# Optimization experiments

Measured on AMD Instinct MI355X. Metric: run time of the kernel, lower is better.

Reference implementation:

```python
import jax, jax.numpy as jnp
import numpy as np

B, C = 16, 256          # batch, feature_dim
P, K = 20, 50           # max_polygons, max_points
H4 = W4 = 32            # p4 spatial
H2 = W2 = 128           # p2 spatial


def setup_inputs() -> dict:
    key = jax.random.key(0)
    ks = jax.random.split(key, 12)

    def w(k, shape, fan_in):
        return jax.random.normal(k, shape, jnp.float32) * (1.0 / np.sqrt(fan_in))

    return {
        "p4": jax.random.normal(ks[0], (B, C, H4, W4), jnp.float32),
        "p2": jax.random.normal(ks[1], (B, C, H2, W2), jnp.float32),
        "segmentation": jax.random.uniform(ks[2], (B, 1, H2, W2), dtype=jnp.float32),
        # init_net linears (torch layout: [out, in])
        "W1": w(ks[3], (1024, C * 64), C * 64), "b1": jnp.zeros((1024,), jnp.float32),
        "W2": w(ks[4], (P * K * 2, 1024), 1024), "b2": jnp.zeros((P * K * 2,), jnp.float32),
        # refine_net
        "R1": w(ks[5], (128, C + 2), C + 2), "rb1": jnp.zeros((128,), jnp.float32),
        "R2": w(ks[6], (64, 128), 128), "rb2": jnp.zeros((64,), jnp.float32),
        "R3": w(ks[7], (2, 64), 64), "rb3": jnp.zeros((2,), jnp.float32),
        # validity_net
        "V1": w(ks[8], (128, K * 2), K * 2), "vb1": jnp.zeros((128,), jnp.float32),
        "V2": w(ks[9], (1, 128), 128), "vb2": jnp.zeros((1,), jnp.float32),
    }


def _bilinear_sample(img, xy):
    """F.grid_sample(align_corners=False, padding='zeros') for one image.
    img: [C, H, W]; xy: [N, 2] in [-1, 1] with xy[:, 0]=x (width), xy[:, 1]=y (height).
    Returns [N, C]."""
    Cc, H, W = img.shape
    x = ((xy[:, 0] + 1.0) * W - 1.0) * 0.5
    y = ((xy[:, 1] + 1.0) * H - 1.0) * 0.5
    x0 = jnp.floor(x)
    y0 = jnp.floor(y)
    wx1 = x - x0
    wy1 = y - y0

    def corner(xi, yi, wgt):
        valid = (xi >= 0) & (xi <= W - 1) & (yi >= 0) & (yi <= H - 1)
        xc = jnp.clip(xi, 0, W - 1).astype(jnp.int32)
        yc = jnp.clip(yi, 0, H - 1).astype(jnp.int32)
        v = img[:, yc, xc]  # [C, N]
        return v * (wgt * valid.astype(img.dtype))[None, :]

    out = (corner(x0, y0, (1 - wx1) * (1 - wy1))
           + corner(x0 + 1, y0, wx1 * (1 - wy1))
           + corner(x0, y0 + 1, (1 - wx1) * wy1)
           + corner(x0 + 1, y0 + 1, wx1 * wy1))
    return out.T  # [N, C]


def reference(p4, p2, segmentation, W1, b1, W2, b2, R1, rb1, R2, rb2, R3, rb3, V1, vb1, V2, vb2):
    Bn, Cc, h4, w4 = p4.shape
    pooled = p4.reshape(Bn, Cc, 8, h4 // 8, 8, w4 // 8).mean(axis=(3, 5))
    flat = pooled.reshape(Bn, -1)                       # [B, C*64]
    h = jax.nn.relu(flat @ W1.T + b1)
    init_pts = jax.nn.sigmoid(h @ W2.T + b2).reshape(Bn, P, K, 2)

    # refine: grid_sample point gather + 3-layer MLP
    grid = init_pts * 2.0 - 1.0                          # [B, P, K, 2]
    xy = grid.reshape(Bn, -1, 2)                         # [B, N=P*K, 2]
    sampled = jax.vmap(_bilinear_sample)(p2, xy)         # [B, N, C]
    coords = init_pts.reshape(Bn, -1, 2)
    feat = jnp.concatenate([sampled, coords], axis=-1)   # [B, N, C+2]
    h1 = jax.nn.relu(feat @ R1.T + rb1)
    h2 = jax.nn.relu(h1 @ R2.T + rb2)
    disp = jnp.tanh(h2 @ R3.T + rb3).reshape(Bn, P, K, 2)
    refined = jnp.clip(init_pts + 0.1 * disp, 0.0, 1.0)

    # validity
    pf = refined.reshape(Bn * P, K * 2)
    v = jax.nn.sigmoid(jax.nn.relu(pf @ V1.T + vb1) @ V2.T + vb2).reshape(Bn, P)
    return refined, v, init_pts
```

## Files before the change

### kernel.cpp

```cpp
#include <hip/hip_runtime.h>
#include <hip/hip_bf16.h>
#include <math.h>

#define NB 16
#define NC 256
#define NPTS 1000
#define NN2 2000
#define D1 1024
#define KFLAT 16384

typedef unsigned short ushort8 __attribute__((ext_vector_type(8)));

static __device__ __forceinline__ float bf2f(unsigned short v) {
    union { unsigned int u; float f; } x;
    x.u = ((unsigned int)v) << 16;
    return x.f;
}

__global__ __launch_bounds__(256) void k_prep(const float* __restrict__ R1,
                                              const float* __restrict__ V1,
                                              float* __restrict__ R1t,
                                              float* __restrict__ V1t_g) {
    int idx = blockIdx.x * 256 + threadIdx.x;
    if (idx < 33024) {
        int j = idx / 258, k = idx % 258;
        R1t[k * 128 + j] = R1[idx];
    } else if (idx < 33024 + 12800) {
        int t = idx - 33024;
        int j = t / 100, k = t % 100;
        V1t_g[k * 128 + j] = V1[t];
    }
}

__global__ __launch_bounds__(256) void k_pool(const float* __restrict__ p4,
                                              __hip_bfloat16* __restrict__ flat_bf) {
    int o = blockIdx.x * 256 + threadIdx.x;
    int bc = o >> 6;
    int ij = o & 63;
    int i = ij >> 3, j = ij & 7;
    const float* src = p4 + ((size_t)bc * 32 + i * 4) * 32 + j * 4;
    float s = 0.f;
#pragma unroll
    for (int di = 0; di < 4; ++di) {
        float4 v = *reinterpret_cast<const float4*>(src + di * 32);
        s += v.x + v.y + v.z + v.w;
    }
    flat_bf[o] = __float2bfloat16(s * (1.0f / 16.0f));
}

__global__ __launch_bounds__(512) void k_fc1(const __hip_bfloat16* __restrict__ flat_bf,
                                             const float* __restrict__ W1,
                                             const float* __restrict__ b1,
                                             float* __restrict__ h) {
    __shared__ unsigned short tile[2 * 16 * 512];
    __shared__ float red[8 * 16];
    const int tid = threadIdx.x;
    const int wave = tid >> 6, lane = tid & 63;
    const int colw = wave & 3, half = wave >> 2;
    const int n = blockIdx.x * 4 + colw;
    float acc[16];
#pragma unroll
    for (int m = 0; m < 16; ++m) acc[m] = 0.f;
    const float4* W1r4 = reinterpret_cast<const float4*>(W1 + (size_t)n * KFLAT + half * 8192);
    const ushort8* flat8 = reinterpret_cast<const ushort8*>(flat_bf);
    ushort8* tile8 = reinterpret_cast<ushort8*>(tile);

    float4 wa = W1r4[lane * 2], wb = W1r4[lane * 2 + 1];
    for (int it = 0; it < 16; ++it) {
        __syncthreads();
#pragma unroll
        for (int r = 0; r < 4; ++r) {
            int idx = tid + r * 512;
            int hh = idx >> 10, m = (idx >> 6) & 15, off = idx & 63;
            tile8[idx] = flat8[m * 2048 + hh * 1024 + it * 64 + off];
        }
        __syncthreads();
        float4 na = wa, nb = wb;
        if (it < 15) {
            na = W1r4[(it + 1) * 128 + lane * 2];
            nb = W1r4[(it + 1) * 128 + lane * 2 + 1];
        }
#pragma unroll
        for (int m = 0; m < 16; ++m) {
            ushort8 u = tile8[half * 1024 + m * 64 + lane];
            float s = wa.x * bf2f(u.s0) + wa.y * bf2f(u.s1)
                    + wa.z * bf2f(u.s2) + wa.w * bf2f(u.s3)
                    + wb.x * bf2f(u.s4) + wb.y * bf2f(u.s5)
                    + wb.z * bf2f(u.s6) + wb.w * bf2f(u.s7);
            acc[m] += s;
        }
        wa = na; wb = nb;
    }
#pragma unroll
    for (int m = 0; m < 16; ++m) {
        float v = acc[m];
#pragma unroll
        for (int off = 32; off > 0; off >>= 1) v += __shfl_xor(v, off, 64);
        acc[m] = v;
    }
    __syncthreads();
    if (lane == 0) {
#pragma unroll
        for (int m = 0; m < 16; ++m) red[wave * 16 + m] = acc[m];
    }
    __syncthreads();
    if (tid < 64) {
        int c = tid >> 4, m = tid & 15;
        float v = red[c * 16 + m] + red[(c + 4) * 16 + m] + b1[blockIdx.x * 4 + c];
        h[m * D1 + blockIdx.x * 4 + c] = fmaxf(v, 0.f);
    }
}

__global__ __launch_bounds__(256) void k_fc2(const float* __restrict__ h,
                                             const float* __restrict__ W2,
                                             const float* __restrict__ b2,
                                             float* __restrict__ init_ws,
                                             float* __restrict__ out_init) {
    const int tid = threadIdx.x;
    const int wave = tid >> 6, lane = tid & 63;
    const int n = blockIdx.x * 4 + wave;
    float acc[16];
#pragma unroll
    for (int m = 0; m < 16; ++m) acc[m] = 0.f;
    const float4* W2r = reinterpret_cast<const float4*>(W2 + (size_t)n * D1);
    const float4* h4  = reinterpret_cast<const float4*>(h);
#pragma unroll
    for (int it = 0; it < 4; ++it) {
        int k4 = it * 64 + lane;
        float4 w = W2r[k4];
#pragma unroll
        for (int m = 0; m < 16; ++m) {
            float4 f = h4[m * 256 + k4];
            acc[m] += w.x * f.x + w.y * f.y + w.z * f.z + w.w * f.w;
        }
    }
    float bias = b2[n];
#pragma unroll
    for (int m = 0; m < 16; ++m) {
        float v = acc[m];
#pragma unroll
        for (int off = 32; off > 0; off >>= 1) v += __shfl_xor(v, off, 64);
        if (lane == 0) {
            float s = 1.f / (1.f + expf(-(v + bias)));
            init_ws[m * NN2 + n] = s;
            out_init[m * NN2 + n] = s;
        }
    }
}

__global__ __launch_bounds__(1024) void k_sample(const float* __restrict__ p2,
                                                 const float* __restrict__ init_ws,
                                                 __hip_bfloat16* __restrict__ sampled) {
    __shared__ float img[128 * 128];
    const int bc = blockIdx.x;
    const int b = bc >> 8;
    const float4* src4 = reinterpret_cast<const float4*>(p2 + (size_t)bc * 16384);
    float4* dst4 = reinterpret_cast<float4*>(img);
#pragma unroll
    for (int i = 0; i < 4; ++i)
        dst4[threadIdx.x + i * 1024] = src4[threadIdx.x + i * 1024];
    __syncthreads();
    const float* ip = init_ws + b * NN2;
    const int n = threadIdx.x;
    if (n < NPTS) {
        float2 sxy = *reinterpret_cast<const float2*>(ip + 2 * n);
        float x = sxy.x * 128.f - 0.5f;
        float y = sxy.y * 128.f - 0.5f;
        float x0f = floorf(x), y0f = floorf(y);
        float wx = x - x0f, wy = y - y0f;
        int x0 = (int)x0f, y0 = (int)y0f;
        int x1 = x0 + 1, y1 = y0 + 1;
        bool vx0 = (x0 >= 0) && (x0 <= 127);
        bool vx1 = (x1 >= 0) && (x1 <= 127);
        bool vy0 = (y0 >= 0) && (y0 <= 127);
        bool vy1 = (y1 >= 0) && (y1 <= 127);
        int cx0 = min(max(x0, 0), 127), cx1 = min(max(x1, 0), 127);
        int cy0 = min(max(y0, 0), 127), cy1 = min(max(y1, 0), 127);
        float v00 = (vx0 && vy0) ? img[cy0 * 128 + cx0] : 0.f;
        float v10 = (vx1 && vy0) ? img[cy0 * 128 + cx1] : 0.f;
        float v01 = (vx0 && vy1) ? img[cy1 * 128 + cx0] : 0.f;
        float v11 = (vx1 && vy1) ? img[cy1 * 128 + cx1] : 0.f;
        float r = v00 * (1.f - wx) * (1.f - wy) + v10 * wx * (1.f - wy)
                + v01 * (1.f - wx) * wy + v11 * wx * wy;
        sampled[(size_t)bc * NPTS + n] = __float2bfloat16(r);
    }
}

__global__ __launch_bounds__(256) void k_r1(const __hip_bfloat16* __restrict__ sampled,
                                            const float* __restrict__ init_ws,
                                            const float* __restrict__ R1t,
                                            const float* __restrict__ rb1,
                                            float* __restrict__ h1t) {
    __shared__ float As[64][128];
    __shared__ float Bs[64][32];
    const int tid = threadIdx.x;
    const int b = blockIdx.x >> 5;
    const int n0 = (blockIdx.x & 31) * 32;
    const int nt = tid & 15;
    const int jt = tid >> 4;
    float acc[8][2];
#pragma unroll
    for (int a = 0; a < 8; ++a) { acc[a][0] = 0.f; acc[a][1] = 0.f; }

    for (int k0 = 0; k0 < 256; k0 += 64) {
        __syncthreads();
        for (int idx = tid; idx < 128 * 64; idx += 256) {
            int kk = idx >> 7, r = idx & 127;
            As[kk][r] = R1t[(k0 + kk) * 128 + r];
        }
        for (int idx = tid; idx < 64 * 32; idx += 256) {
            int r = idx >> 5, col = idx & 31;
            int n = n0 + col;
            Bs[r][col] = (n < NPTS)
                ? __bfloat162float(sampled[((size_t)(b * 256 + k0 + r)) * NPTS + n])
                : 0.f;
        }
        __syncthreads();
#pragma unroll 8
        for (int kk = 0; kk < 64; ++kk) {
            float4 a0 = *reinterpret_cast<const float4*>(&As[kk][jt * 4]);
            float4 a1 = *reinterpret_cast<const float4*>(&As[kk][64 + jt * 4]);
            float2 bb = *reinterpret_cast<const float2*>(&Bs[kk][nt * 2]);
            float av[8] = {a0.x, a0.y, a0.z, a0.w, a1.x, a1.y, a1.z, a1.w};
#pragma unroll
            for (int a = 0; a < 8; ++a) {
                acc[a][0] += av[a] * bb.x;
                acc[a][1] += av[a] * bb.y;
            }
        }
    }
    const int npair = n0 + nt * 2;
    float4 c4 = make_float4(0.f, 0.f, 0.f, 0.f);
    if (npair < NPTS)
        c4 = *reinterpret_cast<const float4*>(init_ws + b * NN2 + 2 * npair);
#pragma unroll
    for (int a = 0; a < 8; ++a) {
        int j = (a < 4) ? (jt * 4 + a) : (64 + jt * 4 + (a - 4));
        float rx = R1t[256 * 128 + j];
        float ry = R1t[257 * 128 + j];
        float bj = rb1[j];
        float v0 = fmaxf(acc[a][0] + rx * c4.x + ry * c4.y + bj, 0.f);
        float v1 = fmaxf(acc[a][1] + rx * c4.z + ry * c4.w + bj, 0.f);
        if (npair < NPTS) {
            float2 st = make_float2(v0, v1);
            *reinterpret_cast<float2*>(h1t + ((size_t)(b * 128 + j)) * NPTS + npair) = st;
        }
    }
}

__global__ __launch_bounds__(512) void k_r23(const float* __restrict__ h1t,
                                             const float* __restrict__ init_ws,
                                             const float* __restrict__ R2,
                                             const float* __restrict__ rb2,
                                             const float* __restrict__ R3,
                                             const float* __restrict__ rb3,
                                             float* __restrict__ refined) {
    __shared__ float hbuf[128][64];
    __shared__ float part[8][2][64];
    const int tid = threadIdx.x;
    const int wave = tid >> 6, lane = tid & 63;
    const int b = blockIdx.x >> 4;
    const int n0 = (blockIdx.x & 15) * 64;
    const int nc = min(n0 + lane, NPTS - 1);

    const float* hsrc = h1t + (size_t)b * (128 * NPTS) + nc;
#pragma unroll
    for (int i = 0; i < 16; ++i) {
        int r = wave * 16 + i;
        hbuf[r][lane] = hsrc[(size_t)r * NPTS];
    }
    __syncthreads();

    const int jb = __builtin_amdgcn_readfirstlane(wave * 8);
    float acc[8];
#pragma unroll
    for (int jj = 0; jj < 8; ++jj) acc[jj] = rb2[jb + jj];
#pragma unroll 4
    for (int k = 0; k < 128; ++k) {
        float hv = hbuf[k][lane];
#pragma unroll
        for (int jj = 0; jj < 8; ++jj)
            acc[jj] = fmaf(R2[(jb + jj) * 128 + k], hv, acc[jj]);
    }
    float d0 = 0.f, d1 = 0.f;
#pragma unroll
    for (int jj = 0; jj < 8; ++jj) {
        float a = fmaxf(acc[jj], 0.f);
        d0 = fmaf(R3[jb + jj], a, d0);
        d1 = fmaf(R3[64 + jb + jj], a, d1);
    }
    part[wave][0][lane] = d0;
    part[wave][1][lane] = d1;
    __syncthreads();
    if (tid < 64) {
        float s0 = 0.f, s1 = 0.f;
#pragma unroll
        for (int w = 0; w < 8; ++w) { s0 += part[w][0][tid]; s1 += part[w][1][tid]; }
        float2 ip = *reinterpret_cast<const float2*>(init_ws + b * NN2 + 2 * nc);
        float rx = fminf(fmaxf(ip.x + 0.1f * tanhf(s0 + rb3[0]), 0.f), 1.f);
        float ry = fminf(fmaxf(ip.y + 0.1f * tanhf(s1 + rb3[1]), 0.f), 1.f);
        if (n0 + tid < NPTS) {
            *reinterpret_cast<float2*>(refined + ((size_t)b * NPTS + n0 + tid) * 2)
                = make_float2(rx, ry);
        }
    }
}

__global__ __launch_bounds__(256) void k_vhead(const float* __restrict__ refined,
                                               const float* __restrict__ V1t_g,
                                               const float* __restrict__ vb1,
                                               const float* __restrict__ V2,
                                               const float* __restrict__ vb2,
                                               float* __restrict__ vout) {
    __shared__ float V1t[100][128];
    __shared__ float pf[4][100];
    const int tid = threadIdx.x, wave = tid >> 6, lane = tid & 63;
    for (int idx = tid; idx < 100 * 128; idx += 256)
        V1t[idx >> 7][idx & 127] = V1t_g[idx];
    __syncthreads();
    const int row = blockIdx.x * 4 + wave;
    const float* src = refined + row * 100;
    if (lane < 50) {
        pf[wave][lane] = src[lane];
        pf[wave][lane + 50] = src[lane + 50];
    }
    __syncthreads();
    float a0 = vb1[lane], a1 = vb1[64 + lane];
#pragma unroll 10
    for (int k = 0; k < 100; ++k) {
        float p = pf[wave][k];
        a0 += V1t[k][lane] * p;
        a1 += V1t[k][64 + lane] * p;
    }
    float s = fmaxf(a0, 0.f) * V2[lane] + fmaxf(a1, 0.f) * V2[64 + lane];
#pragma unroll
    for (int off = 32; off > 0; off >>= 1) s += __shfl_xor(s, off, 64);
    if (lane == 0) vout[row] = 1.f / (1.f + expf(-(s + vb2[0])));
}

extern "C" void kernel_launch(void* const* d_in, const int* in_sizes, int n_in,
                              void* d_out, int out_size, void* d_ws, size_t ws_size,
                              hipStream_t stream) {
    const float* p4  = (const float*)d_in[0];
    const float* p2  = (const float*)d_in[1];
    const float* W1  = (const float*)d_in[3];
    const float* b1  = (const float*)d_in[4];
    const float* W2  = (const float*)d_in[5];
    const float* b2  = (const float*)d_in[6];
    const float* R1  = (const float*)d_in[7];
    const float* rb1 = (const float*)d_in[8];
    const float* R2  = (const float*)d_in[9];
    const float* rb2 = (const float*)d_in[10];
    const float* R3  = (const float*)d_in[11];
    const float* rb3 = (const float*)d_in[12];
    const float* V1  = (const float*)d_in[13];
    const float* vb1 = (const float*)d_in[14];
    const float* V2  = (const float*)d_in[15];
    const float* vb2 = (const float*)d_in[16];
    float* out = (float*)d_out;

    char* ws = (char*)d_ws;
    __hip_bfloat16* flat_bf = (__hip_bfloat16*)(ws + 0);
    float* h    = (float*)(ws + 524288);
    float* ipts = (float*)(ws + 589824);
    float* h1t  = (float*)(ws + 717824);
    __hip_bfloat16* samp = (__hip_bfloat16*)(ws + 8909824);
    float* R1t  = (float*)(ws + 17101824);
    float* V1t_g= (float*)(ws + 17233920);

    k_prep<<<180, 256, 0, stream>>>(R1, V1, R1t, V1t_g);
    k_pool<<<1024, 256, 0, stream>>>(p4, flat_bf);
    k_fc1<<<256, 512, 0, stream>>>(flat_bf, W1, b1, h);
    k_fc2<<<500, 256, 0, stream>>>(h, W2, b2, ipts, out + 32320);
    k_sample<<<4096, 1024, 0, stream>>>(p2, ipts, samp);
    k_r1<<<512, 256, 0, stream>>>(samp, ipts, R1t, rb1, h1t);
    k_r23<<<256, 512, 0, stream>>>(h1t, ipts, R2, rb2, R3, rb3, out);
    k_vhead<<<80, 256, 0, stream>>>(out, V1t_g, vb1, V2, vb2, out + 32000);
}
```

Baseline: 526.6 us.

## Fuse refine MLP layers into one kernel and merge pooling with weight prep

Combines the first refine layer GEMM with the second/third layers so the 128-wide hidden activations stay in shared memory instead of a global h1t buffer. Tiles grow to 64 points per block with vectorized bf16 loads. Also merges the weight transpose kernel into the pooling kernel to drop a launch. Trades fewer blocks (256) and more work per block against removed global traffic and launches.

```diff
diff --git a/kernel.cpp b/kernel.cpp
--- a/kernel.cpp
+++ b/kernel.cpp
@@ -17,35 +17,36 @@
     return x.f;
 }
 
-__global__ __launch_bounds__(256) void k_prep(const float* __restrict__ R1,
-                                              const float* __restrict__ V1,
-                                              float* __restrict__ R1t,
-                                              float* __restrict__ V1t_g) {
+__global__ __launch_bounds__(256) void k_poolprep(const float* __restrict__ p4,
+                                                  const float* __restrict__ R1,
+                                                  const float* __restrict__ V1,
+                                                  __hip_bfloat16* __restrict__ flat_bf,
+                                                  float* __restrict__ R1t,
+                                                  float* __restrict__ V1t_g) {
     int idx = blockIdx.x * 256 + threadIdx.x;
-    if (idx < 33024) {
-        int j = idx / 258, k = idx % 258;
-        R1t[k * 128 + j] = R1[idx];
-    } else if (idx < 33024 + 12800) {
-        int t = idx - 33024;
-        int j = t / 100, k = t % 100;
-        V1t_g[k * 128 + j] = V1[t];
-    }
-}
-
-__global__ __launch_bounds__(256) void k_pool(const float* __restrict__ p4,
-                                              __hip_bfloat16* __restrict__ flat_bf) {
-    int o = blockIdx.x * 256 + threadIdx.x;
-    int bc = o >> 6;
-    int ij = o & 63;
-    int i = ij >> 3, j = ij & 7;
-    const float* src = p4 + ((size_t)bc * 32 + i * 4) * 32 + j * 4;
-    float s = 0.f;
-#pragma unroll
-    for (int di = 0; di < 4; ++di) {
-        float4 v = *reinterpret_cast<const float4*>(src + di * 32);
-        s += v.x + v.y + v.z + v.w;
-    }
-    flat_bf[o] = __float2bfloat16(s * (1.0f / 16.0f));
+    if (idx < 262144) {
+        int bc = idx >> 6;
+        int ij = idx & 63;
+        int i = ij >> 3, j = ij & 7;
+        const float* src = p4 + ((size_t)bc * 32 + i * 4) * 32 + j * 4;
+        float s = 0.f;
+#pragma unroll
+        for (int di = 0; di < 4; ++di) {
+            float4 v = *reinterpret_cast<const float4*>(src + di * 32);
+            s += v.x + v.y + v.z + v.w;
+        }
+        flat_bf[idx] = __float2bfloat16(s * (1.0f / 16.0f));
+    } else {
+        int t = idx - 262144;
+        if (t < 33024) {
+            int j = t / 258, k = t % 258;
+            R1t[k * 128 + j] = R1[t];
+        } else if (t < 33024 + 12800) {
+            int t2 = t - 33024;
+            int j = t2 / 100, k = t2 % 100;
+            V1t_g[k * 128 + j] = V1[t2];
+        }
+    }
 }
 
 __global__ __launch_bounds__(512) void k_fc1(const __hip_bfloat16* __restrict__ flat_bf,
@@ -186,121 +187,127 @@
     }
 }
 
-__global__ __launch_bounds__(256) void k_r1(const __hip_bfloat16* __restrict__ sampled,
-                                            const float* __restrict__ init_ws,
-                                            const float* __restrict__ R1t,
-                                            const float* __restrict__ rb1,
-                                            float* __restrict__ h1t) {
-    __shared__ float As[64][128];
-    __shared__ float Bs[64][32];
+__global__ __launch_bounds__(256) void k_refine(const __hip_bfloat16* __restrict__ sampled,
+                                                const float* __restrict__ init_ws,
+                                                const float* __restrict__ R1t,
+                                                const float* __restrict__ rb1,
+                                                const float* __restrict__ R2,
+                                                const float* __restrict__ rb2,
+                                                const float* __restrict__ R3,
+                                                const float* __restrict__ rb3,
+                                                float* __restrict__ refined) {
+    __shared__ float smem[12288];
     const int tid = threadIdx.x;
-    const int b = blockIdx.x >> 5;
-    const int n0 = (blockIdx.x & 31) * 32;
+    const int b = blockIdx.x >> 4;
+    const int n0 = (blockIdx.x & 15) * 64;
+    const int jt = tid >> 4;
     const int nt = tid & 15;
-    const int jt = tid >> 4;
-    float acc[8][2];
-#pragma unroll
-    for (int a = 0; a < 8; ++a) { acc[a][0] = 0.f; acc[a][1] = 0.f; }
+    float acc[8][4];
+#pragma unroll
+    for (int a = 0; a < 8; ++a)
+#pragma unroll
+        for (int c = 0; c < 4; ++c) acc[a][c] = 0.f;
+
+    const float4* R1t4 = reinterpret_cast<const float4*>(R1t);
+    float4* As4 = reinterpret_cast<float4*>(smem);
 
     for (int k0 = 0; k0 < 256; k0 += 64) {
         __syncthreads();
-        for (int idx = tid; idx < 128 * 64; idx += 256) {
-            int kk = idx >> 7, r = idx & 127;
-            As[kk][r] = R1t[(k0 + kk) * 128 + r];
-        }
-        for (int idx = tid; idx < 64 * 32; idx += 256) {
-            int r = idx >> 5, col = idx & 31;
-            int n = n0 + col;
-            Bs[r][col] = (n < NPTS)
-                ? __bfloat162float(sampled[((size_t)(b * 256 + k0 + r)) * NPTS + n])
-                : 0.f;
+#pragma unroll
+        for (int i = 0; i < 8; ++i) {
+            int idx4 = tid + i * 256;
+            As4[idx4] = R1t4[k0 * 32 + idx4];
+        }
+#pragma unroll
+        for (int c2 = 0; c2 < 2; ++c2) {
+            int chunk = tid + c2 * 256;
+            int row = chunk >> 3, off = chunk & 7;
+            int nb = n0 + off * 8;
+            float4 f0 = make_float4(0.f, 0.f, 0.f, 0.f);
+            float4 f1 = make_float4(0.f, 0.f, 0.f, 0.f);
+            if (nb + 8 <= NPTS) {
+                ushort8 u = *reinterpret_cast<const ushort8*>(
+                    reinterpret_cast<const unsigned short*>(sampled)
+                    + ((size_t)(b * 256 + k0 + row)) * NPTS + nb);
+                f0 = make_float4(bf2f(u.s0), bf2f(u.s1), bf2f(u.s2), bf2f(u.s3));
+                f1 = make_float4(bf2f(u.s4), bf2f(u.s5), bf2f(u.s6), bf2f(u.s7));
+            }
+            float* bp = &smem[8192 + row * 64 + off * 8];
+            *reinterpret_cast<float4*>(bp) = f0;
+            *reinterpret_cast<float4*>(bp + 4) = f1;
         }
         __syncthreads();
-#pragma unroll 8
+#pragma unroll 4
         for (int kk = 0; kk < 64; ++kk) {
-            float4 a0 = *reinterpret_cast<const float4*>(&As[kk][jt * 4]);
-            float4 a1 = *reinterpret_cast<const float4*>(&As[kk][64 + jt * 4]);
-            float2 bb = *reinterpret_cast<const float2*>(&Bs[kk][nt * 2]);
+            const float* Ar = &smem[kk * 128];
+            const float* Br = &smem[8192 + kk * 64];
+            float4 a0 = *reinterpret_cast<const float4*>(Ar + jt * 4);
+            float4 a1 = *reinterpret_cast<const float4*>(Ar + 64 + jt * 4);
+            float4 bb = *reinterpret_cast<const float4*>(Br + nt * 4);
             float av[8] = {a0.x, a0.y, a0.z, a0.w, a1.x, a1.y, a1.z, a1.w};
-#pragma unroll
-            for (int a = 0; a < 8; ++a) {
-                acc[a][0] += av[a] * bb.x;
-                acc[a][1] += av[a] * bb.y;
-            }
-        }
-    }
-    const int npair = n0 + nt * 2;
-    float4 c4 = make_float4(0.f, 0.f, 0.f, 0.f);
-    if (npair < NPTS)
-        c4 = *reinterpret_cast<const float4*>(init_ws + b * NN2 + 2 * npair);
+            float bv[4] = {bb.x, bb.y, bb.z, bb.w};
+#pragma unroll
+            for (int a = 0; a < 8; ++a)
+#pragma unroll
+                for (int c = 0; c < 4; ++c)
+                    acc[a][c] = fmaf(av[a], bv[c], acc[a][c]);
+        }
+    }
+    const int nbase = n0 + nt * 4;
+    float4 cA = *reinterpret_cast<const float4*>(init_ws + b * NN2 + 2 * nbase);
+    float4 cB = *reinterpret_cast<const float4*>(init_ws + b * NN2 + 2 * nbase + 4);
+    __syncthreads();
 #pragma unroll
     for (int a = 0; a < 8; ++a) {
         int j = (a < 4) ? (jt * 4 + a) : (64 + jt * 4 + (a - 4));
         float rx = R1t[256 * 128 + j];
         float ry = R1t[257 * 128 + j];
         float bj = rb1[j];
-        float v0 = fmaxf(acc[a][0] + rx * c4.x + ry * c4.y + bj, 0.f);
-        float v1 = fmaxf(acc[a][1] + rx * c4.z + ry * c4.w + bj, 0.f);
-        if (npair < NPTS) {
-            float2 st = make_float2(v0, v1);
-            *reinterpret_cast<float2*>(h1t + ((size_t)(b * 128 + j)) * NPTS + npair) = st;
-        }
-    }
-}
-
-__global__ __launch_bounds__(512) void k_r23(const float* __restrict__ h1t,
-                                             const float* __restrict__ init_ws,
-                                             const float* __restrict__ R2,
-                                             const float* __restrict__ rb2,
-                                             const float* __restrict__ R3,
-                                             const float* __restrict__ rb3,
-                                             float* __restrict__ refined) {
-    __shared__ float hbuf[128][64];
-    __shared__ float part[8][2][64];
-    const int tid = threadIdx.x;
+        float4 hv;
+        hv.x = fmaxf(acc[a][0] + rx * cA.x + ry * cA.y + bj, 0.f);
+        hv.y = fmaxf(acc[a][1] + rx * cA.z + ry * cA.w + bj, 0.f);
+        hv.z = fmaxf(acc[a][2] + rx * cB.x + ry * cB.y + bj, 0.f);
+        hv.w = fmaxf(acc[a][3] + rx * cB.z + ry * cB.w + bj, 0.f);
+        *reinterpret_cast<float4*>(&smem[j * 64 + nt * 4]) = hv;
+    }
+    __syncthreads();
     const int wave = tid >> 6, lane = tid & 63;
-    const int b = blockIdx.x >> 4;
-    const int n0 = (blockIdx.x & 15) * 64;
-    const int nc = min(n0 + lane, NPTS - 1);
-
-    const float* hsrc = h1t + (size_t)b * (128 * NPTS) + nc;
-#pragma unroll
-    for (int i = 0; i < 16; ++i) {
-        int r = wave * 16 + i;
-        hbuf[r][lane] = hsrc[(size_t)r * NPTS];
-    }
-    __syncthreads();
-
-    const int jb = __builtin_amdgcn_readfirstlane(wave * 8);
-    float acc[8];
-#pragma unroll
-    for (int jj = 0; jj < 8; ++jj) acc[jj] = rb2[jb + jj];
+    const int jb = __builtin_amdgcn_readfirstlane(wave * 16);
+    float a2[16];
+#pragma unroll
+    for (int jj = 0; jj < 16; ++jj) a2[jj] = rb2[jb + jj];
 #pragma unroll 4
     for (int k = 0; k < 128; ++k) {
-        float hv = hbuf[k][lane];
-#pragma unroll
-        for (int jj = 0; jj < 8; ++jj)
-            acc[jj] = fmaf(R2[(jb + jj) * 128 + k], hv, acc[jj]);
+        float hv = smem[k * 64 + lane];
+#pragma unroll
+        for (int jj = 0; jj < 16; ++jj)
+            a2[jj] = fmaf(R2[(jb + jj) * 128 + k], hv, a2[jj]);
     }
     float d0 = 0.f, d1 = 0.f;
 #pragma unroll
-    for (int jj = 0; jj < 8; ++jj) {
-        float a = fmaxf(acc[jj], 0.f);
+    for (int jj = 0; jj < 16; ++jj) {
+        float a = fmaxf(a2[jj], 0.f);
         d0 = fmaf(R3[jb + jj], a, d0);
         d1 = fmaf(R3[64 + jb + jj], a, d1);
     }
-    part[wave][0][lane] = d0;
-    part[wave][1][lane] = d1;
+    float* part = &smem[8192];
+    part[(wave * 2 + 0) * 64 + lane] = d0;
+    part[(wave * 2 + 1) * 64 + lane] = d1;
     __syncthreads();
     if (tid < 64) {
         float s0 = 0.f, s1 = 0.f;
 #pragma unroll
-        for (int w = 0; w < 8; ++w) { s0 += part[w][0][tid]; s1 += part[w][1][tid]; }
+        for (int w = 0; w < 4; ++w) {
+            s0 += part[(w * 2 + 0) * 64 + tid];
+            s1 += part[(w * 2 + 1) * 64 + tid];
+        }
+        int n = n0 + tid;
+        int nc = min(n, NPTS - 1);
         float2 ip = *reinterpret_cast<const float2*>(init_ws + b * NN2 + 2 * nc);
         float rx = fminf(fmaxf(ip.x + 0.1f * tanhf(s0 + rb3[0]), 0.f), 1.f);
         float ry = fminf(fmaxf(ip.y + 0.1f * tanhf(s1 + rb3[1]), 0.f), 1.f);
-        if (n0 + tid < NPTS) {
-            *reinterpret_cast<float2*>(refined + ((size_t)b * NPTS + n0 + tid) * 2)
+        if (n < NPTS) {
+            *reinterpret_cast<float2*>(refined + ((size_t)b * NPTS + n) * 2)
                 = make_float2(rx, ry);
         }
     }
@@ -363,17 +370,14 @@
     __hip_bfloat16* flat_bf = (__hip_bfloat16*)(ws + 0);
     float* h    = (float*)(ws + 524288);
     float* ipts = (float*)(ws + 589824);
-    float* h1t  = (float*)(ws + 717824);
-    __hip_bfloat16* samp = (__hip_bfloat16*)(ws + 8909824);
-    float* R1t  = (float*)(ws + 17101824);
-    float* V1t_g= (float*)(ws + 17233920);
-
-    k_prep<<<180, 256, 0, stream>>>(R1, V1, R1t, V1t_g);
-    k_pool<<<1024, 256, 0, stream>>>(p4, flat_bf);
+    __hip_bfloat16* samp = (__hip_bfloat16*)(ws + 717824);
+    float* R1t  = (float*)(ws + 8909824);
+    float* V1t_g= (float*)(ws + 9041920);
+
+    k_poolprep<<<1204, 256, 0, stream>>>(p4, R1, V1, flat_bf, R1t, V1t_g);
     k_fc1<<<256, 512, 0, stream>>>(flat_bf, W1, b1, h);
     k_fc2<<<500, 256, 0, stream>>>(h, W2, b2, ipts, out + 32320);
     k_sample<<<4096, 1024, 0, stream>>>(p2, ipts, samp);
-    k_r1<<<512, 256, 0, stream>>>(samp, ipts, R1t, rb1, h1t);
-    k_r23<<<256, 512, 0, stream>>>(h1t, ipts, R2, rb2, R3, rb3, out);
+    k_refine<<<256, 256, 0, stream>>>(samp, ipts, R1t, rb1, R2, rb2, R3, rb3, out);
     k_vhead<<<80, 256, 0, stream>>>(out, V1t_g, vb1, V2, vb2, out + 32000);
 }
```

Measured after the change: 510.7 us. 1.03x faster.
